# Kernel optimization log

Measured on AMD Instinct MI355X. Metric: run time of the kernel, lower is better.

## Reference

```python
import jax, jax.numpy as jnp
import numpy as np

EPS = 1e-6
CHI2_THRESH = 9.0
DIST_SCALE = 3.0


def _normalize(x, axis=1, eps=EPS):
    n = jnp.linalg.norm(x, axis=axis, keepdims=True)
    return x / jnp.maximum(n, eps)


def _skew(k):
    # k: (B,3) -> (B,3,3)
    kx, ky, kz = k[:, 0], k[:, 1], k[:, 2]
    O = jnp.zeros_like(kx)
    row0 = jnp.stack([O, -kz, ky], axis=1)
    row1 = jnp.stack([kz, O, -kx], axis=1)
    row2 = jnp.stack([-ky, kx, O], axis=1)
    return jnp.stack([row0, row1, row2], axis=1)


def gravity_align(g_src, g_tgt, eps=EPS):
    # Rodrigues rotation aligning g_src to g_tgt, batch-safe.
    u = _normalize(g_src, eps=eps)
    v = _normalize(g_tgt, eps=eps)
    axis = jnp.cross(u, v)
    axis_norm = jnp.linalg.norm(axis, axis=1, keepdims=True)
    dot = jnp.clip(jnp.sum(u * v, axis=1, keepdims=True), -1.0, 1.0)
    parallel = axis_norm < 1e-6
    k = axis / (axis_norm + eps)
    theta = jnp.arccos(dot)
    sin_t, cos_t = jnp.sin(theta), jnp.cos(theta)
    K = _skew(k)
    I = jnp.eye(3, dtype=g_src.dtype)[None]
    R = I + sin_t[:, :, None] * K + (1.0 - cos_t)[:, :, None] * (K @ K)
    # anti-parallel branch (computed unconditionally, selected via where)
    ex = jnp.array([1.0, 0.0, 0.0], dtype=u.dtype)[None]
    ey = jnp.array([0.0, 1.0, 0.0], dtype=u.dtype)[None]
    use_ex = jnp.abs(u[:, 0:1]) < 0.9
    basis = jnp.where(use_ex, ex, ey)
    axis2 = _normalize(jnp.cross(u, basis), eps=eps)
    K2 = _skew(axis2)
    R_anti = I + 2.0 * (K2 @ K2)
    antipar = parallel & (dot < 0.0)
    R = jnp.where(antipar[:, :, None], R_anti, R)
    R = jnp.where((parallel & (dot > 0.0))[:, :, None], I, R)
    return R


def _lower_median(x, axis):
    # torch.median(dim): lower median for even length
    n = x.shape[axis]
    return jnp.sort(x, axis=axis).take(indices=(n - 1) // 2, axis=axis)


def setup_inputs() -> dict:
    key = jax.random.key(0)
    ks = jax.random.split(key, 8)
    B, N = 4, 4096
    src = jax.random.normal(ks[0], (B, 3, N), jnp.float32)
    tgt = jax.random.normal(ks[1], (B, 3, N), jnp.float32)
    src_n = _normalize(jax.random.normal(ks[2], (B, 3, N), jnp.float32))
    tgt_n = _normalize(jax.random.normal(ks[3], (B, 3, N), jnp.float32))
    g_p = jax.random.normal(ks[4], (B, 3), jnp.float32)
    g_q = jax.random.normal(ks[5], (B, 3), jnp.float32)
    k_p = jax.random.uniform(ks[6], (B, 1), jnp.float32) + 0.1
    k_q = jax.random.uniform(ks[7], (B, 1), jnp.float32) + 0.1
    return {"src": src, "tgt": tgt, "src_n": src_n, "tgt_n": tgt_n,
            "g_p": g_p, "k_p": k_p, "g_q": g_q, "k_q": k_q}


def reference(src, tgt, src_n, tgt_n, g_p, k_p, g_q, k_q):
    B, _, N = src.shape
    R_g = gravity_align(g_p, g_q)  # (B,3,3)
    src_rot = jnp.einsum('bij,bjn->bin', R_g, src)
    src_n_rot = jnp.einsum('bij,bjn->bin', R_g, src_n)
    t_center = tgt.mean(axis=2, keepdims=True) - src_rot.mean(axis=2, keepdims=True)
    src_init = src_rot + t_center  # (B,3,N)

    # squared pairwise distances: (B,N,N)
    inner = -2.0 * jnp.einsum('bcn,bcm->bnm', src_init, tgt)
    xx = jnp.sum(src_init ** 2, axis=1)[:, :, None]
    yy = jnp.sum(tgt ** 2, axis=1)[:, None, :]
    dist_pq = xx + inner + yy

    min_pq = jnp.min(dist_pq, axis=2)
    corr_p2q = jnp.argmin(dist_pq, axis=2)
    min_qp = jnp.min(dist_pq, axis=1)
    corr_q2p = jnp.argmin(dist_pq, axis=1)

    nn_d_p = jnp.sqrt(jnp.maximum(min_pq, 0.0) + EPS)
    nn_d_q = jnp.sqrt(jnp.maximum(min_qp, 0.0) + EPS)
    tau_p = DIST_SCALE * _lower_median(nn_d_p, axis=1)[:, None]
    tau_q = DIST_SCALE * _lower_median(nn_d_q, axis=1)[:, None]
    geom_p = (nn_d_p <= tau_p).astype(src.dtype)
    geom_q = (nn_d_q <= tau_q).astype(src.dtype)

    tgt_n_matched_for_p = jnp.take_along_axis(tgt_n, corr_p2q[:, None, :], axis=2)
    src_n_matched_for_q = jnp.take_along_axis(src_n_rot, corr_q2p[:, None, :], axis=2)

    gq = g_q[:, :, None]
    inc_p = jnp.sum(src_n_rot * gq, axis=1)
    inc_p_ref = jnp.sum(tgt_n_matched_for_p * gq, axis=1)
    inc_q = jnp.sum(tgt_n * gq, axis=1)
    inc_q_ref = jnp.sum(src_n_matched_for_q * gq, axis=1)

    k_eff = k_p * k_q / (k_p + k_q + EPS)  # (B,1), broadcasts over N
    w_p = jax.nn.sigmoid(CHI2_THRESH - k_eff * (inc_p - inc_p_ref) ** 2) * geom_p
    w_q = jax.nn.sigmoid(CHI2_THRESH - k_eff * (inc_q - inc_q_ref) ** 2) * geom_q
    return w_p[:, None, :], w_q[:, None, :]
```

## Files before the change

### kernel.cpp

```cpp
#include <hip/hip_runtime.h>
#include <math.h>

#define NPTS 4096
#define NB 4
#define EPSF 1e-6f

__device__ __forceinline__ void gravity_align_rt(
    const float* __restrict__ g_p, const float* __restrict__ g_q,
    const float* sums, int b, float* R_out, float* t_out) {
    float gpx = g_p[3 * b + 0], gpy = g_p[3 * b + 1], gpz = g_p[3 * b + 2];
    float gqx = g_q[3 * b + 0], gqy = g_q[3 * b + 1], gqz = g_q[3 * b + 2];
    float nu = sqrtf(gpx * gpx + gpy * gpy + gpz * gpz);
    float du = fmaxf(nu, EPSF);
    float ux = gpx / du, uy = gpy / du, uz = gpz / du;
    float nv = sqrtf(gqx * gqx + gqy * gqy + gqz * gqz);
    float dv = fmaxf(nv, EPSF);
    float vx = gqx / dv, vy = gqy / dv, vz = gqz / dv;

    float ax = uy * vz - uz * vy;
    float ay = uz * vx - ux * vz;
    float az = ux * vy - uy * vx;
    float an = sqrtf(ax * ax + ay * ay + az * az);
    float dot = ux * vx + uy * vy + uz * vz;
    dot = fminf(1.0f, fmaxf(-1.0f, dot));
    bool parallel = (an < 1e-6f);

    float kx = ax / (an + EPSF), ky = ay / (an + EPSF), kz = az / (an + EPSF);
    float theta = acosf(dot);
    float st = sinf(theta), ct = cosf(theta);

    float K[9] = {0.f, -kz, ky,  kz, 0.f, -kx,  -ky, kx, 0.f};
    float KK[9];
    for (int i = 0; i < 3; ++i)
        for (int j = 0; j < 3; ++j) {
            float s2 = 0.f;
            for (int l = 0; l < 3; ++l) s2 += K[i * 3 + l] * K[l * 3 + j];
            KK[i * 3 + j] = s2;
        }
    float R[9];
    for (int i = 0; i < 9; ++i) {
        float I = (i == 0 || i == 4 || i == 8) ? 1.f : 0.f;
        R[i] = I + st * K[i] + (1.f - ct) * KK[i];
    }
    if (parallel) {
        if (dot < 0.f) {
            float bx, by, bz;
            if (fabsf(ux) < 0.9f) { bx = 1.f; by = 0.f; bz = 0.f; }
            else                  { bx = 0.f; by = 1.f; bz = 0.f; }
            float cx = uy * bz - uz * by;
            float cy = uz * bx - ux * bz;
            float cz = ux * by - uy * bx;
            float cn = sqrtf(cx * cx + cy * cy + cz * cz);
            float cd = fmaxf(cn, EPSF);
            cx /= cd; cy /= cd; cz /= cd;
            float K2[9] = {0.f, -cz, cy,  cz, 0.f, -cx,  -cy, cx, 0.f};
            float K2K2[9];
            for (int i = 0; i < 3; ++i)
                for (int j = 0; j < 3; ++j) {
                    float s2 = 0.f;
                    for (int l = 0; l < 3; ++l) s2 += K2[i * 3 + l] * K2[l * 3 + j];
                    K2K2[i * 3 + j] = s2;
                }
            for (int i = 0; i < 9; ++i) {
                float I = (i == 0 || i == 4 || i == 8) ? 1.f : 0.f;
                R[i] = I + 2.f * K2K2[i];
            }
        } else if (dot > 0.f) {
            for (int i = 0; i < 9; ++i) R[i] = (i == 0 || i == 4 || i == 8) ? 1.f : 0.f;
        }
    }
    float ms0 = sums[0] / (float)NPTS, ms1 = sums[1] / (float)NPTS, ms2 = sums[2] / (float)NPTS;
    float mt0 = sums[3] / (float)NPTS, mt1 = sums[4] / (float)NPTS, mt2 = sums[5] / (float)NPTS;
    for (int i = 0; i < 9; ++i) R_out[i] = R[i];
    t_out[0] = mt0 - (R[0] * ms0 + R[1] * ms1 + R[2] * ms2);
    t_out[1] = mt1 - (R[3] * ms0 + R[4] * ms1 + R[5] * ms2);
    t_out[2] = mt2 - (R[6] * ms0 + R[7] * ms1 + R[8] * ms2);
}

__global__ void k0a_rt(const float* __restrict__ src, const float* __restrict__ tgt,
                       const float* __restrict__ g_p, const float* __restrict__ g_q,
                       float* __restrict__ Rt) {
    const int b = blockIdx.x;
    const int tid = threadIdx.x;
    const float* S = src + (size_t)b * 3 * NPTS;
    const float* T = tgt + (size_t)b * 3 * NPTS;

    float acc[6] = {0.f, 0.f, 0.f, 0.f, 0.f, 0.f};
    for (int n = tid; n < NPTS; n += 256) {
        acc[0] += S[n]; acc[1] += S[NPTS + n]; acc[2] += S[2 * NPTS + n];
        acc[3] += T[n]; acc[4] += T[NPTS + n]; acc[5] += T[2 * NPTS + n];
    }
    __shared__ float red[256];
    __shared__ float sums[6];
    for (int c = 0; c < 6; ++c) {
        red[tid] = acc[c];
        __syncthreads();
        for (int s = 128; s > 0; s >>= 1) {
            if (tid < s) red[tid] += red[tid + s];
            __syncthreads();
        }
        if (tid == 0) sums[c] = red[0];
        __syncthreads();
    }
    if (tid == 0) {
        float Rg[9], tc[3];
        gravity_align_rt(g_p, g_q, sums, b, Rg, tc);
        for (int i = 0; i < 9; ++i) Rt[b * 16 + i] = Rg[i];
        Rt[b * 16 + 9]  = tc[0];
        Rt[b * 16 + 10] = tc[1];
        Rt[b * 16 + 11] = tc[2];
    }
}

__global__ void k1r(const float* __restrict__ src, const float* __restrict__ tgt,
                    const float* __restrict__ Rt,
                    float* __restrict__ nnp, int* __restrict__ idxp,
                    float* __restrict__ nnq, int* __restrict__ idxq) {
    const int b = blockIdx.y;
    const int z = blockIdx.z;
    const int tid = threadIdx.x;
    const float* S = src + (size_t)b * 3 * NPTS;
    const float* T = tgt + (size_t)b * 3 * NPTS;
    const float R0 = Rt[b*16+0], R1 = Rt[b*16+1], R2 = Rt[b*16+2];
    const float R3 = Rt[b*16+3], R4 = Rt[b*16+4], R5 = Rt[b*16+5];
    const float R6 = Rt[b*16+6], R7 = Rt[b*16+7], R8 = Rt[b*16+8];
    const float t0 = Rt[b*16+9], t1 = Rt[b*16+10], t2 = Rt[b*16+11];

    __shared__ float4 stage4[NPTS];
    const int nl = tid & 63;
    const int stripe = tid >> 6;
    const int n = blockIdx.x * 64 + nl;
    float4 p;

    if (z == 0) {
        for (int i = tid; i < NPTS; i += 1024) {
            float q0 = T[i], q1 = T[NPTS + i], q2 = T[2 * NPTS + i];
            float w = (q0 * q0 + q1 * q1 + q2 * q2) * -0.5f;
            stage4[i] = make_float4(q0, q1, q2, w);
        }
        float s0 = S[n], s1 = S[NPTS + n], s2 = S[2 * NPTS + n];
        float p0 = R0 * s0 + R1 * s1 + R2 * s2 + t0;
        float p1 = R3 * s0 + R4 * s1 + R5 * s2 + t1;
        float p2 = R6 * s0 + R7 * s1 + R8 * s2 + t2;
        p = make_float4(p0, p1, p2, p0 * p0 + p1 * p1 + p2 * p2);
    } else {
        for (int i = tid; i < NPTS; i += 1024) {
            float s0 = S[i], s1 = S[NPTS + i], s2 = S[2 * NPTS + i];
            float p0 = R0 * s0 + R1 * s1 + R2 * s2 + t0;
            float p1 = R3 * s0 + R4 * s1 + R5 * s2 + t1;
            float p2 = R6 * s0 + R7 * s1 + R8 * s2 + t2;
            float w = (p0 * p0 + p1 * p1 + p2 * p2) * -0.5f;
            stage4[i] = make_float4(p0, p1, p2, w);
        }
        float q0 = T[n], q1 = T[NPTS + n], q2 = T[2 * NPTS + n];
        p = make_float4(q0, q1, q2, q0 * q0 + q1 * q1 + q2 * q2);
    }
    __syncthreads();

    const int m0 = stripe << 8;
    float best = -3.4e38f;
    int bi = m0;
    #pragma unroll 8
    for (int m = m0; m < m0 + 256; ++m) {
        float4 q = stage4[m];
        float s = fmaf(p.x, q.x, fmaf(p.y, q.y, fmaf(p.z, q.z, q.w)));
        if (s > best) { best = s; bi = m; }
    }
    __syncthreads();

    float* combd = (float*)stage4;
    int* combi = (int*)(combd + 1024);
    combd[tid] = best;
    combi[tid] = bi;
    __syncthreads();
    if (stripe == 0) {
        for (int s2 = 1; s2 < 16; ++s2) {
            float d2 = combd[s2 * 64 + nl];
            int i2 = combi[s2 * 64 + nl];
            if (d2 > best) { best = d2; bi = i2; }
        }
        float d = fmaf(-2.0f, best, p.w);
        float* nn = z ? nnq : nnp;
        int* idx = z ? idxq : idxp;
        nn[b * NPTS + n] = sqrtf(fmaxf(d, 0.f) + EPSF);
        idx[b * NPTS + n] = bi;
    }
}

__global__ void kcr(const float* __restrict__ nnp, const float* __restrict__ nnq,
                    const int* __restrict__ idxp, const int* __restrict__ idxq,
                    const float* __restrict__ src_n, const float* __restrict__ tgt_n,
                    const float* __restrict__ Rt,
                    const float* __restrict__ g_q, const float* __restrict__ k_p,
                    const float* __restrict__ k_q, float* __restrict__ out) {
    const int x = blockIdx.x;
    const int b = blockIdx.y;
    const int z = blockIdx.z;
    const int tid = threadIdx.x;
    const int wid = tid >> 6;
    const int lane = tid & 63;
    const float* a = (z ? nnq : nnp) + b * NPTS;

    unsigned int v[4];
    #pragma unroll
    for (int j = 0; j < 4; ++j)
        v[j] = __float_as_uint(a[tid + j * 1024]);

    __shared__ int hist[16][256];
    __shared__ int tot[256];
    __shared__ int digit_s, base_s;

    const int shifts[4]   = {23, 15, 7, 0};
    const unsigned him[4] = {0x00000000u, 0x7F800000u, 0x7FFF8000u, 0x7FFFFF80u};
    const unsigned dm[4]  = {0xFFu, 0xFFu, 0xFFu, 0x7Fu};

    unsigned int prefix = 0u;
    int rank = 2047;

    for (int p = 0; p < 4; ++p) {
        const int sh = shifts[p];
        const unsigned himask = him[p];
        const unsigned dmask = dm[p];

        for (int k2 = lane; k2 < 256; k2 += 64) hist[wid][k2] = 0;
        __syncthreads();

        #pragma unroll
        for (int j = 0; j < 4; ++j) {
            if ((v[j] & himask) == prefix)
                atomicAdd(&hist[wid][(v[j] >> sh) & dmask], 1);
        }
        __syncthreads();

        if (tid < 256) {
            int t = 0;
            #pragma unroll
            for (int w = 0; w < 16; ++w) t += hist[w][tid];
            tot[tid] = t;
        }
        __syncthreads();

        if (wid == 0) {
            int c0 = tot[4 * lane + 0], c1 = tot[4 * lane + 1];
            int c2 = tot[4 * lane + 2], c3 = tot[4 * lane + 3];
            int s = c0 + c1 + c2 + c3;
            int incl = s;
            #pragma unroll
            for (int o = 1; o < 64; o <<= 1) {
                int t = __shfl_up(incl, o, 64);
                if (lane >= o) incl += t;
            }
            int base = incl - s;
            int cs[4] = {c0, c1, c2, c3};
            #pragma unroll
            for (int k2 = 0; k2 < 4; ++k2) {
                if (cs[k2] > 0 && rank >= base && rank < base + cs[k2]) {
                    digit_s = 4 * lane + k2;
                    base_s = base;
                }
                base += cs[k2];
            }
        }
        __syncthreads();
        prefix |= ((unsigned)digit_s) << sh;
        rank -= base_s;
        __syncthreads();
    }
    const float tauv = 3.0f * __uint_as_float(prefix);

    if (tid < 64) {
        const int n = x * 64 + tid;
        const float* SN = src_n + (size_t)b * 3 * NPTS;
        const float* TN = tgt_n + (size_t)b * 3 * NPTS;
        const float R0 = Rt[b*16+0], R1 = Rt[b*16+1], R2 = Rt[b*16+2];
        const float R3 = Rt[b*16+3], R4 = Rt[b*16+4], R5 = Rt[b*16+5];
        const float R6 = Rt[b*16+6], R7 = Rt[b*16+7], R8 = Rt[b*16+8];
        const float gx = g_q[3 * b + 0], gy = g_q[3 * b + 1], gz = g_q[3 * b + 2];
        const float kp = k_p[b], kq = k_q[b];
        const float keff = kp * kq / (kp + kq + EPSF);

        float w;
        if (z == 0) {
            float a0 = SN[n], a1 = SN[NPTS + n], a2 = SN[2 * NPTS + n];
            float snx = R0 * a0 + R1 * a1 + R2 * a2;
            float sny = R3 * a0 + R4 * a1 + R5 * a2;
            float snz = R6 * a0 + R7 * a1 + R8 * a2;
            float inc = snx * gx + sny * gy + snz * gz;
            int jj = idxp[b * NPTS + n];
            float tnx = TN[jj], tny = TN[NPTS + jj], tnz = TN[2 * NPTS + jj];
            float incr = tnx * gx + tny * gy + tnz * gz;
            float diff = inc - incr;
            float arg = 9.0f - keff * diff * diff;
            float sig = 1.f / (1.f + expf(-arg));
            float geom = (a[n] <= tauv) ? 1.f : 0.f;
            w = sig * geom;
        } else {
            float tnx = TN[n], tny = TN[NPTS + n], tnz = TN[2 * NPTS + n];
            float inc = tnx * gx + tny * gy + tnz * gz;
            int jj = idxq[b * NPTS + n];
            float a0 = SN[jj], a1 = SN[NPTS + jj], a2 = SN[2 * NPTS + jj];
            float snx = R0 * a0 + R1 * a1 + R2 * a2;
            float sny = R3 * a0 + R4 * a1 + R5 * a2;
            float snz = R6 * a0 + R7 * a1 + R8 * a2;
            float incr = snx * gx + sny * gy + snz * gz;
            float diff = inc - incr;
            float arg = 9.0f - keff * diff * diff;
            float sig = 1.f / (1.f + expf(-arg));
            float geom = (a[n] <= tauv) ? 1.f : 0.f;
            w = sig * geom;
        }
        out[z * (NB * NPTS) + b * NPTS + n] = w;
    }
}

extern "C" void kernel_launch(void* const* d_in, const int* in_sizes, int n_in,
                              void* d_out, int out_size, void* d_ws, size_t ws_size,
                              hipStream_t stream) {
    const float* src   = (const float*)d_in[0];
    const float* tgt   = (const float*)d_in[1];
    const float* src_n = (const float*)d_in[2];
    const float* tgt_n = (const float*)d_in[3];
    const float* g_p   = (const float*)d_in[4];
    const float* k_p   = (const float*)d_in[5];
    const float* g_q   = (const float*)d_in[6];
    const float* k_q   = (const float*)d_in[7];
    float* out = (float*)d_out;

    const int BN = NB * NPTS;
    float* nnp = (float*)d_ws;
    float* nnq = nnp + BN;
    int* idxp = (int*)(nnq + BN);
    int* idxq = idxp + BN;
    float* Rt  = (float*)(idxq + BN);

    k0a_rt<<<dim3(NB), dim3(256), 0, stream>>>(src, tgt, g_p, g_q, Rt);
    k1r<<<dim3(NPTS / 64, NB, 2), dim3(1024), 0, stream>>>(src, tgt, Rt,
                                                           nnp, idxp, nnq, idxq);
    kcr<<<dim3(NPTS / 64, NB, 2), dim3(1024), 0, stream>>>(nnp, nnq, idxp, idxq,
                                                           src_n, tgt_n, Rt,
                                                           g_q, k_p, k_q, out);
}
```

Measured before the change: 46.55 us.

## Fuse rigid-transform computation into NN and weight kernels, drop separate launch

Removes the single-purpose k0a_rt kernel and instead recomputes the per-batch means and gravity-aligned rotation/translation redundantly inside every block of both the NN kernel and the weight kernel, via a shared-memory reduction. This eliminates one kernel launch and the serial dependency on a tiny 4-block kernel. In exchange each of the 512 blocks per kernel re-reads 24K floats of src/tgt and performs an extra reduction with several barriers. Launch bounds are also added.

Measured after the change: 47.88 us. +2.8%, slower.

```diff
diff --git a/kernel.cpp b/kernel.cpp
--- a/kernel.cpp
+++ b/kernel.cpp
@@ -77,56 +77,59 @@
     t_out[2] = mt2 - (R[6] * ms0 + R[7] * ms1 + R[8] * ms2);
 }
 
-__global__ void k0a_rt(const float* __restrict__ src, const float* __restrict__ tgt,
-                       const float* __restrict__ g_p, const float* __restrict__ g_q,
-                       float* __restrict__ Rt) {
-    const int b = blockIdx.x;
-    const int tid = threadIdx.x;
-    const float* S = src + (size_t)b * 3 * NPTS;
-    const float* T = tgt + (size_t)b * 3 * NPTS;
-
+__device__ __forceinline__ void block_means_rt(
+    const float* __restrict__ S, const float* __restrict__ T,
+    const float* __restrict__ g_p, const float* __restrict__ g_q,
+    int b, int tid, float* sf) {
     float acc[6] = {0.f, 0.f, 0.f, 0.f, 0.f, 0.f};
-    for (int n = tid; n < NPTS; n += 256) {
-        acc[0] += S[n]; acc[1] += S[NPTS + n]; acc[2] += S[2 * NPTS + n];
-        acc[3] += T[n]; acc[4] += T[NPTS + n]; acc[5] += T[2 * NPTS + n];
-    }
-    __shared__ float red[256];
-    __shared__ float sums[6];
-    for (int c = 0; c < 6; ++c) {
-        red[tid] = acc[c];
-        __syncthreads();
-        for (int s = 128; s > 0; s >>= 1) {
-            if (tid < s) red[tid] += red[tid + s];
-            __syncthreads();
-        }
-        if (tid == 0) sums[c] = red[0];
+    if (tid < 256) {
+        for (int n = tid; n < NPTS; n += 256) {
+            acc[0] += S[n]; acc[1] += S[NPTS + n]; acc[2] += S[2 * NPTS + n];
+            acc[3] += T[n]; acc[4] += T[NPTS + n]; acc[5] += T[2 * NPTS + n];
+        }
+    }
+    if (tid < 256) {
+        #pragma unroll
+        for (int c = 0; c < 6; ++c) sf[c * 256 + tid] = acc[c];
+    }
+    __syncthreads();
+    for (int s = 128; s > 0; s >>= 1) {
+        if (tid < s) {
+            #pragma unroll
+            for (int c = 0; c < 6; ++c) sf[c * 256 + tid] += sf[c * 256 + tid + s];
+        }
         __syncthreads();
     }
     if (tid == 0) {
-        float Rg[9], tc[3];
-        gravity_align_rt(g_p, g_q, sums, b, Rg, tc);
-        for (int i = 0; i < 9; ++i) Rt[b * 16 + i] = Rg[i];
-        Rt[b * 16 + 9]  = tc[0];
-        Rt[b * 16 + 10] = tc[1];
-        Rt[b * 16 + 11] = tc[2];
-    }
-}
-
-__global__ void k1r(const float* __restrict__ src, const float* __restrict__ tgt,
-                    const float* __restrict__ Rt,
-                    float* __restrict__ nnp, int* __restrict__ idxp,
-                    float* __restrict__ nnq, int* __restrict__ idxq) {
+        float sums[6];
+        #pragma unroll
+        for (int c = 0; c < 6; ++c) sums[c] = sf[c * 256];
+        gravity_align_rt(g_p, g_q, sums, b, sf + 1536, sf + 1545);
+    }
+    __syncthreads();
+}
+
+__global__ __launch_bounds__(1024, 8) void kA(
+    const float* __restrict__ src, const float* __restrict__ tgt,
+    const float* __restrict__ g_p, const float* __restrict__ g_q,
+    float* __restrict__ nnp, int* __restrict__ idxp,
+    float* __restrict__ nnq, int* __restrict__ idxq) {
     const int b = blockIdx.y;
     const int z = blockIdx.z;
     const int tid = threadIdx.x;
     const float* S = src + (size_t)b * 3 * NPTS;
     const float* T = tgt + (size_t)b * 3 * NPTS;
-    const float R0 = Rt[b*16+0], R1 = Rt[b*16+1], R2 = Rt[b*16+2];
-    const float R3 = Rt[b*16+3], R4 = Rt[b*16+4], R5 = Rt[b*16+5];
-    const float R6 = Rt[b*16+6], R7 = Rt[b*16+7], R8 = Rt[b*16+8];
-    const float t0 = Rt[b*16+9], t1 = Rt[b*16+10], t2 = Rt[b*16+11];
 
     __shared__ float4 stage4[NPTS];
+    float* sf = (float*)stage4;
+
+    block_means_rt(S, T, g_p, g_q, b, tid, sf);
+    const float R0 = sf[1536], R1 = sf[1537], R2 = sf[1538];
+    const float R3 = sf[1539], R4 = sf[1540], R5 = sf[1541];
+    const float R6 = sf[1542], R7 = sf[1543], R8 = sf[1544];
+    const float t0 = sf[1545], t1 = sf[1546], t2 = sf[1547];
+    __syncthreads();
+
     const int nl = tid & 63;
     const int stripe = tid >> 6;
     const int n = blockIdx.x * 64 + nl;
@@ -168,7 +171,7 @@
     }
     __syncthreads();
 
-    float* combd = (float*)stage4;
+    float* combd = sf;
     int* combi = (int*)(combd + 1024);
     combd[tid] = best;
     combi[tid] = bi;
@@ -187,28 +190,38 @@
     }
 }
 
-__global__ void kcr(const float* __restrict__ nnp, const float* __restrict__ nnq,
-                    const int* __restrict__ idxp, const int* __restrict__ idxq,
-                    const float* __restrict__ src_n, const float* __restrict__ tgt_n,
-                    const float* __restrict__ Rt,
-                    const float* __restrict__ g_q, const float* __restrict__ k_p,
-                    const float* __restrict__ k_q, float* __restrict__ out) {
+__global__ __launch_bounds__(1024, 8) void kB(
+    const float* __restrict__ src, const float* __restrict__ tgt,
+    const float* __restrict__ nnp, const float* __restrict__ nnq,
+    const int* __restrict__ idxp, const int* __restrict__ idxq,
+    const float* __restrict__ src_n, const float* __restrict__ tgt_n,
+    const float* __restrict__ g_p, const float* __restrict__ g_q,
+    const float* __restrict__ k_p, const float* __restrict__ k_q,
+    float* __restrict__ out) {
     const int x = blockIdx.x;
     const int b = blockIdx.y;
     const int z = blockIdx.z;
     const int tid = threadIdx.x;
     const int wid = tid >> 6;
     const int lane = tid & 63;
+    const float* S = src + (size_t)b * 3 * NPTS;
+    const float* T = tgt + (size_t)b * 3 * NPTS;
     const float* a = (z ? nnq : nnp) + b * NPTS;
+
+    __shared__ float msc[1548];
+    __shared__ int hist[16][256];
+    __shared__ int tot[256];
+    __shared__ int digit_s, base_s;
+
+    block_means_rt(S, T, g_p, g_q, b, tid, msc);
+    const float R0 = msc[1536], R1 = msc[1537], R2 = msc[1538];
+    const float R3 = msc[1539], R4 = msc[1540], R5 = msc[1541];
+    const float R6 = msc[1542], R7 = msc[1543], R8 = msc[1544];
 
     unsigned int v[4];
     #pragma unroll
     for (int j = 0; j < 4; ++j)
         v[j] = __float_as_uint(a[tid + j * 1024]);
-
-    __shared__ int hist[16][256];
-    __shared__ int tot[256];
-    __shared__ int digit_s, base_s;
 
     const int shifts[4]   = {23, 15, 7, 0};
     const unsigned him[4] = {0x00000000u, 0x7F800000u, 0x7FFF8000u, 0x7FFFFF80u};
@@ -272,9 +285,6 @@
         const int n = x * 64 + tid;
         const float* SN = src_n + (size_t)b * 3 * NPTS;
         const float* TN = tgt_n + (size_t)b * 3 * NPTS;
-        const float R0 = Rt[b*16+0], R1 = Rt[b*16+1], R2 = Rt[b*16+2];
-        const float R3 = Rt[b*16+3], R4 = Rt[b*16+4], R5 = Rt[b*16+5];
-        const float R6 = Rt[b*16+6], R7 = Rt[b*16+7], R8 = Rt[b*16+8];
         const float gx = g_q[3 * b + 0], gy = g_q[3 * b + 1], gz = g_q[3 * b + 2];
         const float kp = k_p[b], kq = k_q[b];
         const float keff = kp * kq / (kp + kq + EPSF);
@@ -331,12 +341,10 @@
     float* nnq = nnp + BN;
     int* idxp = (int*)(nnq + BN);
     int* idxq = idxp + BN;
-    float* Rt  = (float*)(idxq + BN);
-
-    k0a_rt<<<dim3(NB), dim3(256), 0, stream>>>(src, tgt, g_p, g_q, Rt);
-    k1r<<<dim3(NPTS / 64, NB, 2), dim3(1024), 0, stream>>>(src, tgt, Rt,
-                                                           nnp, idxp, nnq, idxq);
-    kcr<<<dim3(NPTS / 64, NB, 2), dim3(1024), 0, stream>>>(nnp, nnq, idxp, idxq,
-                                                           src_n, tgt_n, Rt,
-                                                           g_q, k_p, k_q, out);
-}
+
+    kA<<<dim3(NPTS / 64, NB, 2), dim3(1024), 0, stream>>>(src, tgt, g_p, g_q,
+                                                          nnp, idxp, nnq, idxq);
+    kB<<<dim3(NPTS / 64, NB, 2), dim3(1024), 0, stream>>>(src, tgt, nnp, nnq,
+                                                          idxp, idxq, src_n, tgt_n,
+                                                          g_p, g_q, k_p, k_q, out);
+}
```

## Split NN search over target quarters with 4-query register blocking per thread

Applied to the files above, without the earlier changes.

The nearest-neighbour kernel now gives each block 256 query points (4 per thread, held in registers) and only a quarter of the candidate set staged in shared memory. Each shared-memory load is therefore reused across four queries. Partial maxima from the four quarters are written to workspace, and the median/weight kernel merges them before computing distances and the histogram median. This cuts shared staging and LDS traffic per comparison and shrinks per-block shared memory, at the cost of extra global writes and reads for the partial results and redundant merges in the second kernel.

After: 47.76 us. 1.03x slower.

```diff
diff --git a/kernel.cpp b/kernel.cpp
--- a/kernel.cpp
+++ b/kernel.cpp
@@ -112,12 +112,16 @@
     }
 }
 
-__global__ void k1r(const float* __restrict__ src, const float* __restrict__ tgt,
-                    const float* __restrict__ Rt,
-                    float* __restrict__ nnp, int* __restrict__ idxp,
-                    float* __restrict__ nnq, int* __restrict__ idxq) {
+__global__ __launch_bounds__(1024, 8) void kA(
+    const float* __restrict__ src, const float* __restrict__ tgt,
+    const float* __restrict__ Rt,
+    float* __restrict__ bestv, int* __restrict__ bidx,
+    float* __restrict__ pw) {
+    const int x = blockIdx.x;
     const int b = blockIdx.y;
-    const int z = blockIdx.z;
+    const int zz = blockIdx.z;
+    const int z = zz >> 2;
+    const int q = zz & 3;
     const int tid = threadIdx.x;
     const float* S = src + (size_t)b * 3 * NPTS;
     const float* T = tgt + (size_t)b * 3 * NPTS;
@@ -126,85 +130,121 @@
     const float R6 = Rt[b*16+6], R7 = Rt[b*16+7], R8 = Rt[b*16+8];
     const float t0 = Rt[b*16+9], t1 = Rt[b*16+10], t2 = Rt[b*16+11];
 
-    __shared__ float4 stage4[NPTS];
+    __shared__ float4 buf[2048];
+    float4* stage4 = buf;
+    const int mbase = q * 1024;
+
     const int nl = tid & 63;
     const int stripe = tid >> 6;
-    const int n = blockIdx.x * 64 + nl;
-    float4 p;
+    const int n0 = x * 256 + nl;
+    float4 p[4];
 
     if (z == 0) {
-        for (int i = tid; i < NPTS; i += 1024) {
-            float q0 = T[i], q1 = T[NPTS + i], q2 = T[2 * NPTS + i];
+        if (tid < 1024) {
+            const int gi = mbase + tid;
+            float q0 = T[gi], q1 = T[NPTS + gi], q2 = T[2 * NPTS + gi];
             float w = (q0 * q0 + q1 * q1 + q2 * q2) * -0.5f;
-            stage4[i] = make_float4(q0, q1, q2, w);
-        }
-        float s0 = S[n], s1 = S[NPTS + n], s2 = S[2 * NPTS + n];
-        float p0 = R0 * s0 + R1 * s1 + R2 * s2 + t0;
-        float p1 = R3 * s0 + R4 * s1 + R5 * s2 + t1;
-        float p2 = R6 * s0 + R7 * s1 + R8 * s2 + t2;
-        p = make_float4(p0, p1, p2, p0 * p0 + p1 * p1 + p2 * p2);
+            stage4[tid] = make_float4(q0, q1, q2, w);
+        }
+        #pragma unroll
+        for (int k = 0; k < 4; ++k) {
+            const int n = n0 + 64 * k;
+            float s0 = S[n], s1 = S[NPTS + n], s2 = S[2 * NPTS + n];
+            float p0 = R0 * s0 + R1 * s1 + R2 * s2 + t0;
+            float p1 = R3 * s0 + R4 * s1 + R5 * s2 + t1;
+            float p2 = R6 * s0 + R7 * s1 + R8 * s2 + t2;
+            p[k] = make_float4(p0, p1, p2, p0 * p0 + p1 * p1 + p2 * p2);
+        }
     } else {
-        for (int i = tid; i < NPTS; i += 1024) {
-            float s0 = S[i], s1 = S[NPTS + i], s2 = S[2 * NPTS + i];
+        if (tid < 1024) {
+            const int gi = mbase + tid;
+            float s0 = S[gi], s1 = S[NPTS + gi], s2 = S[2 * NPTS + gi];
             float p0 = R0 * s0 + R1 * s1 + R2 * s2 + t0;
             float p1 = R3 * s0 + R4 * s1 + R5 * s2 + t1;
             float p2 = R6 * s0 + R7 * s1 + R8 * s2 + t2;
             float w = (p0 * p0 + p1 * p1 + p2 * p2) * -0.5f;
-            stage4[i] = make_float4(p0, p1, p2, w);
-        }
-        float q0 = T[n], q1 = T[NPTS + n], q2 = T[2 * NPTS + n];
-        p = make_float4(q0, q1, q2, q0 * q0 + q1 * q1 + q2 * q2);
+            stage4[tid] = make_float4(p0, p1, p2, w);
+        }
+        #pragma unroll
+        for (int k = 0; k < 4; ++k) {
+            const int n = n0 + 64 * k;
+            float q0 = T[n], q1 = T[NPTS + n], q2 = T[2 * NPTS + n];
+            p[k] = make_float4(q0, q1, q2, q0 * q0 + q1 * q1 + q2 * q2);
+        }
     }
     __syncthreads();
 
-    const int m0 = stripe << 8;
-    float best = -3.4e38f;
-    int bi = m0;
+    const int m0 = stripe << 6;
+    float best[4] = {-3.4e38f, -3.4e38f, -3.4e38f, -3.4e38f};
+    int bi[4] = {m0, m0, m0, m0};
     #pragma unroll 8
-    for (int m = m0; m < m0 + 256; ++m) {
-        float4 q = stage4[m];
-        float s = fmaf(p.x, q.x, fmaf(p.y, q.y, fmaf(p.z, q.z, q.w)));
-        if (s > best) { best = s; bi = m; }
+    for (int m = m0; m < m0 + 64; ++m) {
+        float4 qq = stage4[m];
+        #pragma unroll
+        for (int k = 0; k < 4; ++k) {
+            float s = fmaf(p[k].x, qq.x, fmaf(p[k].y, qq.y, fmaf(p[k].z, qq.z, qq.w)));
+            if (s > best[k]) { best[k] = s; bi[k] = m; }
+        }
     }
     __syncthreads();
 
-    float* combd = (float*)stage4;
-    int* combi = (int*)(combd + 1024);
-    combd[tid] = best;
-    combi[tid] = bi;
+    float* combd = (float*)buf;
+    int* combi = (int*)((float*)buf + 4096);
+    #pragma unroll
+    for (int k = 0; k < 4; ++k) {
+        combd[k * 1024 + tid] = best[k];
+        combi[k * 1024 + tid] = bi[k];
+    }
     __syncthreads();
     if (stripe == 0) {
-        for (int s2 = 1; s2 < 16; ++s2) {
-            float d2 = combd[s2 * 64 + nl];
-            int i2 = combi[s2 * 64 + nl];
-            if (d2 > best) { best = d2; bi = i2; }
-        }
-        float d = fmaf(-2.0f, best, p.w);
-        float* nn = z ? nnq : nnp;
-        int* idx = z ? idxq : idxp;
-        nn[b * NPTS + n] = sqrtf(fmaxf(d, 0.f) + EPSF);
-        idx[b * NPTS + n] = bi;
-    }
-}
-
-__global__ void kcr(const float* __restrict__ nnp, const float* __restrict__ nnq,
-                    const int* __restrict__ idxp, const int* __restrict__ idxq,
-                    const float* __restrict__ src_n, const float* __restrict__ tgt_n,
-                    const float* __restrict__ Rt,
-                    const float* __restrict__ g_q, const float* __restrict__ k_p,
-                    const float* __restrict__ k_q, float* __restrict__ out) {
+        #pragma unroll
+        for (int k = 0; k < 4; ++k) {
+            float bk = best[k];
+            int ik = bi[k];
+            for (int s2 = 1; s2 < 16; ++s2) {
+                float d2 = combd[k * 1024 + s2 * 64 + nl];
+                int i2 = combi[k * 1024 + s2 * 64 + nl];
+                if (d2 > bk) { bk = d2; ik = i2; }
+            }
+            const size_t off = (size_t)(z * NB + b) * NPTS;
+            const int n = n0 + 64 * k;
+            bestv[(size_t)q * (2 * NB * NPTS) + off + n] = bk;
+            bidx[(size_t)q * (2 * NB * NPTS) + off + n] = mbase + ik;
+            if (q == 0) pw[off + n] = p[k].w;
+        }
+    }
+}
+
+__global__ __launch_bounds__(1024, 8) void kB(
+    const float* __restrict__ bestv, const int* __restrict__ bidx,
+    const float* __restrict__ pw,
+    const float* __restrict__ src_n, const float* __restrict__ tgt_n,
+    const float* __restrict__ Rt,
+    const float* __restrict__ g_q, const float* __restrict__ k_p,
+    const float* __restrict__ k_q, float* __restrict__ out) {
     const int x = blockIdx.x;
     const int b = blockIdx.y;
     const int z = blockIdx.z;
     const int tid = threadIdx.x;
     const int wid = tid >> 6;
     const int lane = tid & 63;
-    const float* a = (z ? nnq : nnp) + b * NPTS;
+    const size_t off = (size_t)(z * NB + b) * NPTS;
+    const size_t QS = (size_t)2 * NB * NPTS;
 
     unsigned int v[4];
     #pragma unroll
-    for (int j = 0; j < 4; ++j)
-        v[j] = __float_as_uint(a[tid + j * 1024]);
+    for (int j = 0; j < 4; ++j) {
+        const int n = tid + j * 1024;
+        float sb = bestv[off + n];
+        #pragma unroll
+        for (int qq = 1; qq < 4; ++qq) {
+            float sq = bestv[(size_t)qq * QS + off + n];
+            if (sq > sb) sb = sq;
+        }
+        float d = fmaf(-2.0f, sb, pw[off + n]);
+        float nv = sqrtf(fmaxf(d, 0.f) + EPSF);
+        v[j] = __float_as_uint(nv);
+    }
 
     __shared__ int hist[16][256];
     __shared__ int tot[256];
@@ -270,6 +310,16 @@
 
     if (tid < 64) {
         const int n = x * 64 + tid;
+        float sb = bestv[off + n];
+        int jj = bidx[off + n];
+        #pragma unroll
+        for (int qq = 1; qq < 4; ++qq) {
+            float sq = bestv[(size_t)qq * QS + off + n];
+            if (sq > sb) { sb = sq; jj = bidx[(size_t)qq * QS + off + n]; }
+        }
+        float d = fmaf(-2.0f, sb, pw[off + n]);
+        float nv = sqrtf(fmaxf(d, 0.f) + EPSF);
+
         const float* SN = src_n + (size_t)b * 3 * NPTS;
         const float* TN = tgt_n + (size_t)b * 3 * NPTS;
         const float R0 = Rt[b*16+0], R1 = Rt[b*16+1], R2 = Rt[b*16+2];
@@ -286,18 +336,16 @@
             float sny = R3 * a0 + R4 * a1 + R5 * a2;
             float snz = R6 * a0 + R7 * a1 + R8 * a2;
             float inc = snx * gx + sny * gy + snz * gz;
-            int jj = idxp[b * NPTS + n];
             float tnx = TN[jj], tny = TN[NPTS + jj], tnz = TN[2 * NPTS + jj];
             float incr = tnx * gx + tny * gy + tnz * gz;
             float diff = inc - incr;
             float arg = 9.0f - keff * diff * diff;
             float sig = 1.f / (1.f + expf(-arg));
-            float geom = (a[n] <= tauv) ? 1.f : 0.f;
+            float geom = (nv <= tauv) ? 1.f : 0.f;
             w = sig * geom;
         } else {
             float tnx = TN[n], tny = TN[NPTS + n], tnz = TN[2 * NPTS + n];
             float inc = tnx * gx + tny * gy + tnz * gz;
-            int jj = idxq[b * NPTS + n];
             float a0 = SN[jj], a1 = SN[NPTS + jj], a2 = SN[2 * NPTS + jj];
             float snx = R0 * a0 + R1 * a1 + R2 * a2;
             float sny = R3 * a0 + R4 * a1 + R5 * a2;
@@ -306,7 +354,7 @@
             float diff = inc - incr;
             float arg = 9.0f - keff * diff * diff;
             float sig = 1.f / (1.f + expf(-arg));
-            float geom = (a[n] <= tauv) ? 1.f : 0.f;
+            float geom = (nv <= tauv) ? 1.f : 0.f;
             w = sig * geom;
         }
         out[z * (NB * NPTS) + b * NPTS + n] = w;
@@ -326,17 +374,15 @@
     const float* k_q   = (const float*)d_in[7];
     float* out = (float*)d_out;
 
-    const int BN = NB * NPTS;
-    float* nnp = (float*)d_ws;
-    float* nnq = nnp + BN;
-    int* idxp = (int*)(nnq + BN);
-    int* idxq = idxp + BN;
-    float* Rt  = (float*)(idxq + BN);
+    const size_t QS = (size_t)2 * NB * NPTS;
+    float* bestv = (float*)d_ws;
+    int* bidx = (int*)(bestv + 4 * QS);
+    float* pw = (float*)(bidx + 4 * QS);
+    float* Rt = pw + QS;
 
     k0a_rt<<<dim3(NB), dim3(256), 0, stream>>>(src, tgt, g_p, g_q, Rt);
-    k1r<<<dim3(NPTS / 64, NB, 2), dim3(1024), 0, stream>>>(src, tgt, Rt,
-                                                           nnp, idxp, nnq, idxq);
-    kcr<<<dim3(NPTS / 64, NB, 2), dim3(1024), 0, stream>>>(nnp, nnq, idxp, idxq,
-                                                           src_n, tgt_n, Rt,
-                                                           g_q, k_p, k_q, out);
-}
+    kA<<<dim3(16, NB, 8), dim3(1024), 0, stream>>>(src, tgt, Rt, bestv, bidx, pw);
+    kB<<<dim3(NPTS / 64, NB, 2), dim3(1024), 0, stream>>>(bestv, bidx, pw,
+                                                          src_n, tgt_n, Rt,
+                                                          g_q, k_p, k_q, out);
+}
```
